# Optimization experiments

Measured on AMD Instinct MI355X. Metric: run time of the kernel, lower is better.

The kernel has to match this reference:

```python
import jax, jax.numpy as jnp
import numpy as np

B, S, D, H = 2, 4096, 512, 8
DK = D // H


def setup_inputs() -> dict:
    key = jax.random.key(0)
    ks = jax.random.split(key, 8)
    q = jax.random.normal(ks[0], (B, S, D), dtype=jnp.float32)
    k = jax.random.normal(ks[1], (B, S, D), dtype=jnp.float32)
    v = jax.random.normal(ks[2], (B, S, D), dtype=jnp.float32)
    mask = jax.random.randint(ks[3], (B, S, S), 0, 2, dtype=jnp.int32)
    scale = 1.0 / np.sqrt(D)
    w_q = jax.random.normal(ks[4], (D, D), dtype=jnp.float32) * scale
    w_k = jax.random.normal(ks[5], (D, D), dtype=jnp.float32) * scale
    w_v = jax.random.normal(ks[6], (D, D), dtype=jnp.float32) * scale
    w_o = jax.random.normal(ks[7], (D, D), dtype=jnp.float32) * scale
    return {"q": q, "k": k, "v": v, "mask": mask,
            "w_q": w_q, "w_k": w_k, "w_v": w_v, "w_o": w_o}


def reference(q, k, v, mask, w_q, w_k, w_v, w_o):
    # Projections (weights stored as [in, out]; no bias, matching bias=False)
    # [B,S,D] -> [B,H,S,DK]
    def split_heads(x):
        return x.reshape(B, S, H, DK).transpose(0, 2, 1, 3)

    qh = split_heads(q @ w_q)
    kh = split_heads(k @ w_k)
    vh = split_heads(v @ w_v)

    inv_sqrt_dk = jnp.float32(1.0 / np.sqrt(DK))
    # Explicit O(S^2) score matrix, as in the original module
    scores = jnp.einsum('bhqd,bhkd->bhqk', qh, kh) * inv_sqrt_dk
    scores = jnp.where(mask[:, None, :, :] == 0, jnp.float32(-1e9), scores)
    attn = jax.nn.softmax(scores, axis=-1)
    # dropout in eval mode (p=0) -> identity
    x = jnp.einsum('bhqk,bhkd->bhqd', attn, vh)
    x = x.transpose(0, 2, 1, 3).reshape(B, S, D)
    return x @ w_o
```

## Files before the change

### kernel.cpp

```cpp
#include <hip/hip_runtime.h>
#include <hip/hip_bf16.h>

#define Bn 2
#define Sn 4096
#define Dn 512
#define Hn 8
#define DKn 64

typedef __attribute__((ext_vector_type(8))) short bf16x8;
typedef __attribute__((ext_vector_type(4))) float f32x4;
typedef __attribute__((ext_vector_type(4))) _Float16 f16x4;
typedef __attribute__((ext_vector_type(8))) unsigned short us8;
typedef __attribute__((ext_vector_type(4))) unsigned short us4;

__device__ __forceinline__ unsigned short f2bf(float f) {
  unsigned u = __builtin_bit_cast(unsigned, f);
  u += 0x7fffu + ((u >> 16) & 1u);
  return (unsigned short)(u >> 16);
}

__global__ __launch_bounds__(256) void pack_mask_k(const int* __restrict__ mask,
                                                   unsigned int* __restrict__ pm) {
  int gid = blockIdx.x * 256 + threadIdx.x;
  int m = mask[gid];
  unsigned long long bal = __ballot(m != 0);
  if ((threadIdx.x & 63) == 0) {
    int q = (gid >> 12) & 4095;
    int b = gid >> 24;
    int kvw = (gid >> 5) & 127;
    pm[((size_t)b * 128 + kvw) * 4096 + q] = (unsigned)bal;
    pm[((size_t)b * 128 + kvw + 1) * 4096 + q] = (unsigned)(bal >> 32);
  }
}

__global__ __launch_bounds__(256) void cvt_k(const float* __restrict__ q,
                                             const float* __restrict__ k,
                                             const float* __restrict__ v,
                                             unsigned short* __restrict__ o) {
  const float* src = blockIdx.y == 0 ? q : blockIdx.y == 1 ? k : v;
  size_t i = (size_t)blockIdx.x * 256 + threadIdx.x;
  float4 f = *(const float4*)&src[i * 4];
  us4 r = {f2bf(f.x), f2bf(f.y), f2bf(f.z), f2bf(f.w)};
  *(us4*)&o[(size_t)blockIdx.y * (Bn * Sn * Dn) + i * 4] = r;
}

__global__ __launch_bounds__(256) void wt_k(const float* __restrict__ wq,
                                            const float* __restrict__ wk,
                                            const float* __restrict__ wv,
                                            const float* __restrict__ wo,
                                            unsigned short* __restrict__ wt) {
  __shared__ unsigned short ls[64][68];
  const float* W = blockIdx.z == 0 ? wq : blockIdx.z == 1 ? wk
                 : blockIdx.z == 2 ? wv : wo;
  int k0 = blockIdx.x * 64, n0 = blockIdx.y * 64;
  int t = threadIdx.x;
  for (int j = 0; j < 4; ++j) {
    int i = t + j * 256;
    int r = i >> 4, c4 = (i & 15) << 2;
    float4 f = *(const float4*)&W[(size_t)(k0 + r) * 512 + n0 + c4];
    ls[c4 + 0][r] = f2bf(f.x);
    ls[c4 + 1][r] = f2bf(f.y);
    ls[c4 + 2][r] = f2bf(f.z);
    ls[c4 + 3][r] = f2bf(f.w);
  }
  __syncthreads();
  unsigned short* out = wt + (size_t)blockIdx.z * 512 * 512;
  for (int j = 0; j < 4; ++j) {
    int i = t + j * 256;
    int r = i >> 4, c4 = (i & 15) << 2;
    us4 v = {ls[r][c4], ls[r][c4 + 1], ls[r][c4 + 2], ls[r][c4 + 3]};
    *(us4*)&out[(size_t)(n0 + r) * 512 + k0 + c4] = v;
  }
}

template <int MT, bool HEADS>
__global__ __launch_bounds__(256, 2) void gemm_k(
    const unsigned short* __restrict__ A0, size_t zstride,
    const unsigned short* __restrict__ wt, unsigned short* __restrict__ oh,
    unsigned short* __restrict__ vtg, float* __restrict__ olin) {
  __shared__ unsigned short As[MT * 64 * 64];
  __shared__ unsigned short Bs[128 * 64];
  const int z = blockIdx.z;
  const unsigned short* A = A0 + zstride * z;
  const unsigned short* Wt = wt + (size_t)z * 512 * 512;
  const float scale = (HEADS && z == 0) ? 0.125f * 1.44269504088896f : 1.0f;
  const int m0 = blockIdx.x * (MT * 64), n0 = blockIdx.y * 128;
  const int t = threadIdx.x, w = t >> 6, l = t & 63;
  const int quad = l >> 4, c = l & 15;

  f32x4 acc[MT][8] = {};

  us8 apre[MT * 2], bpre[4];
#pragma unroll
  for (int j = 0; j < MT * 2; ++j) {
    int i = t + j * 256, r = i >> 3, u = i & 7;
    apre[j] = *(const us8*)&A[(size_t)(m0 + r) * 512 + (u << 3)];
  }
#pragma unroll
  for (int j = 0; j < 4; ++j) {
    int i = t + j * 256, r = i >> 3, u = i & 7;
    bpre[j] = *(const us8*)&Wt[(size_t)(n0 + r) * 512 + (u << 3)];
  }

  for (int k0 = 0; k0 < 512; k0 += 64) {
    __syncthreads();
#pragma unroll
    for (int j = 0; j < MT * 2; ++j) {
      int i = t + j * 256, r = i >> 3, u = i & 7;
      *(us8*)&As[r * 64 + ((u ^ (r & 7)) << 3)] = apre[j];
    }
#pragma unroll
    for (int j = 0; j < 4; ++j) {
      int i = t + j * 256, r = i >> 3, u = i & 7;
      *(us8*)&Bs[r * 64 + ((u ^ (r & 7)) << 3)] = bpre[j];
    }
    __syncthreads();
    if (k0 + 64 < 512) {
#pragma unroll
      for (int j = 0; j < MT * 2; ++j) {
        int i = t + j * 256, r = i >> 3, u = i & 7;
        apre[j] = *(const us8*)&A[(size_t)(m0 + r) * 512 + k0 + 64 + (u << 3)];
      }
#pragma unroll
      for (int j = 0; j < 4; ++j) {
        int i = t + j * 256, r = i >> 3, u = i & 7;
        bpre[j] = *(const us8*)&Wt[(size_t)(n0 + r) * 512 + k0 + 64 + (u << 3)];
      }
    }

#pragma unroll
    for (int kc = 0; kc < 2; ++kc) {
      bf16x8 aA[MT], bB[8];
      int u = kc * 4 + quad;
#pragma unroll
      for (int mt = 0; mt < MT; ++mt) {
        int row = w * (MT * 16) + mt * 16 + c;
        aA[mt] = *(const bf16x8*)&As[row * 64 + ((u ^ (c & 7)) << 3)];
      }
#pragma unroll
      for (int nt = 0; nt < 8; ++nt) {
        int row = nt * 16 + c;
        bB[nt] = *(const bf16x8*)&Bs[row * 64 + ((u ^ (c & 7)) << 3)];
      }
#pragma unroll
      for (int mt = 0; mt < MT; ++mt)
#pragma unroll
        for (int nt = 0; nt < 8; ++nt)
          acc[mt][nt] = __builtin_amdgcn_mfma_f32_16x16x32_bf16(
              aA[mt], bB[nt], acc[mt][nt], 0, 0, 0);
    }
  }

#pragma unroll
  for (int mt = 0; mt < MT; ++mt)
#pragma unroll
    for (int nt = 0; nt < 8; ++nt)
#pragma unroll
      for (int r = 0; r < 4; ++r) {
        int m = m0 + w * (MT * 16) + mt * 16 + (quad << 2) + r;
        int n = n0 + nt * 16 + c;
        float val = acc[mt][nt][r] * scale;
        if constexpr (HEADS) {
          int b = m >> 12, s = m & 4095, h = n >> 6, dk = n & 63;
          if (z < 2) {
            oh[(size_t)z * (Bn * Hn * Sn * DKn) +
               ((size_t)(b * Hn + h) * Sn + s) * DKn + dk] = f2bf(val);
          } else {
            int sl = s & 63;
            int pos = (((sl >> 5) & 1) << 5) | (((sl >> 2) & 3) << 3) |
                      (((sl >> 4) & 1) << 2) | (sl & 3);
            vtg[((size_t)(b * Hn + h) * DKn + dk) * Sn + (s & ~63) + pos] =
                __builtin_bit_cast(unsigned short, (_Float16)val);
          }
        } else {
          olin[(size_t)m * 512 + n] = val;
        }
      }
}

__global__ __launch_bounds__(256, 2) void flash_k(
    const unsigned short* __restrict__ Qh, const unsigned short* __restrict__ Kh,
    const unsigned short* __restrict__ VtG, const unsigned int* __restrict__ pmt,
    unsigned short* __restrict__ attn) {
  __shared__ unsigned short Ks[64 * 64];
  __shared__ unsigned short Vts[64 * 64];
  __shared__ unsigned int Mw[256];

  const int q0 = blockIdx.x * 128, h = blockIdx.y, b = blockIdx.z;
  const int t = threadIdx.x, w = t >> 6, l = t & 63;
  const int quad = l >> 4, c = l & 15;
  const size_t hb = (size_t)(b * Hn + h) * Sn * DKn;
  const unsigned short* Qg = Qh + hb;
  const unsigned short* Kg = Kh + hb;
  const unsigned short* Vg = VtG + hb;

  bf16x8 bQ[2][2];
#pragma unroll
  for (int qf = 0; qf < 2; ++qf) {
    int qrow = q0 + w * 32 + qf * 16 + c;
#pragma unroll
    for (int kc = 0; kc < 2; ++kc)
      bQ[qf][kc] = *(const bf16x8*)&Qg[(size_t)qrow * 64 + kc * 32 + quad * 8];
  }

  f32x4 oacc[2][4] = {};
  float lsum[2] = {};
  const int sr = t >> 3, su = t & 7;

  us8 kpre[2], vpre[2];
  unsigned mpre;
#pragma unroll
  for (int j = 0; j < 2; ++j) {
    kpre[j] = *(const us8*)&Kg[(size_t)(sr + j * 32) * 64 + (su << 3)];
    vpre[j] = *(const us8*)&Vg[(size_t)(sr + j * 32) * Sn + (su << 3)];
  }
  mpre = pmt[((size_t)b * 128 + (t >> 7)) * 4096 + q0 + (t & 127)];

  for (int kv0 = 0; kv0 < Sn; kv0 += 64) {
    __syncthreads();
#pragma unroll
    for (int j = 0; j < 2; ++j) {
      int r = sr + j * 32;
      *(us8*)&Ks[r * 64 + ((su ^ (r & 7)) << 3)] = kpre[j];
      *(us8*)&Vts[r * 64 + ((su ^ (r & 7)) << 3)] = vpre[j];
    }
    Mw[t] = mpre;
    __syncthreads();
    if (kv0 + 64 < Sn) {
#pragma unroll
      for (int j = 0; j < 2; ++j) {
        kpre[j] = *(const us8*)&Kg[(size_t)(kv0 + 64 + sr + j * 32) * 64 + (su << 3)];
        vpre[j] = *(const us8*)&Vg[(size_t)(sr + j * 32) * Sn + kv0 + 64 + (su << 3)];
      }
      mpre = pmt[((size_t)b * 128 + ((kv0 + 64) >> 5) + (t >> 7)) * 4096 +
                 q0 + (t & 127)];
    }

    f32x4 sacc[2][4] = {};
#pragma unroll
    for (int kc = 0; kc < 2; ++kc) {
      int u = kc * 4 + quad;
#pragma unroll
      for (int kvt = 0; kvt < 4; ++kvt) {
        int row = kvt * 16 + c;
        bf16x8 aK = *(const bf16x8*)&Ks[row * 64 + ((u ^ (c & 7)) << 3)];
#pragma unroll
        for (int qf = 0; qf < 2; ++qf)
          sacc[qf][kvt] = __builtin_amdgcn_mfma_f32_16x16x32_bf16(
              aK, bQ[qf][kc], sacc[qf][kvt], 0, 0, 0);
      }
    }

    f16x4 pb[2][4];
#pragma unroll
    for (int qf = 0; qf < 2; ++qf) {
      int qloc = w * 32 + qf * 16 + c;
      unsigned mv0 = Mw[qloc], mv1 = Mw[128 + qloc];
#pragma unroll
      for (int kvt = 0; kvt < 4; ++kvt) {
        unsigned word = (kvt & 2) ? mv1 : mv0;
        unsigned bits = (word >> (((kvt & 1) << 4) + (quad << 2))) & 15u;
        float ps = 0.f;
#pragma unroll
        for (int r = 0; r < 4; ++r) {
          float p = ((bits >> r) & 1u) ? __builtin_amdgcn_exp2f(sacc[qf][kvt][r])
                                       : 0.f;
          ps += p;
          pb[qf][kvt][r] = (_Float16)p;
        }
        lsum[qf] += ps;
      }
    }

#pragma unroll
    for (int kp = 0; kp < 2; ++kp) {
#pragma unroll
      for (int dkt = 0; dkt < 4; ++dkt) {
        int dk = dkt * 16 + c;
        us8 vv = *(const us8*)&Vts[dk * 64 + (((kp * 4 + quad) ^ (c & 7)) << 3)];
        f16x4 lo = __builtin_bit_cast(f16x4, (us4){vv[0], vv[1], vv[2], vv[3]});
        f16x4 hi = __builtin_bit_cast(f16x4, (us4){vv[4], vv[5], vv[6], vv[7]});
#pragma unroll
        for (int qf = 0; qf < 2; ++qf) {
          oacc[qf][dkt] = __builtin_amdgcn_mfma_f32_16x16x16f16(
              pb[qf][kp * 2], lo, oacc[qf][dkt], 0, 0, 0);
          oacc[qf][dkt] = __builtin_amdgcn_mfma_f32_16x16x16f16(
              pb[qf][kp * 2 + 1], hi, oacc[qf][dkt], 0, 0, 0);
        }
      }
    }
  }

#pragma unroll
  for (int qf = 0; qf < 2; ++qf) {
    float s = lsum[qf];
    s += __shfl_xor(s, 16, 64);
    s += __shfl_xor(s, 32, 64);
    float inv = 1.0f / s;
#pragma unroll
    for (int r = 0; r < 4; ++r) {
      float invr = __shfl(inv, (quad << 2) + r, 64);
      unsigned short* dst =
          &attn[((size_t)(b * Sn + q0 + w * 32 + qf * 16 + (quad << 2) + r)) * Dn +
                h * 64 + c];
#pragma unroll
      for (int dkt = 0; dkt < 4; ++dkt)
        dst[dkt * 16] = f2bf(oacc[qf][dkt][r] * invr);
    }
  }
}

extern "C" void kernel_launch(void* const* d_in, const int* in_sizes, int n_in,
                              void* d_out, int out_size, void* d_ws,
                              size_t ws_size, hipStream_t stream) {
  const float* q = (const float*)d_in[0];
  const float* k = (const float*)d_in[1];
  const float* v = (const float*)d_in[2];
  const int* mask = (const int*)d_in[3];
  const float* wq = (const float*)d_in[4];
  const float* wk = (const float*)d_in[5];
  const float* wv = (const float*)d_in[6];
  const float* wo = (const float*)d_in[7];
  float* out = (float*)d_out;

  char* ws = (char*)d_ws;
  const size_t headN = (size_t)Bn * Hn * Sn * DKn;
  const size_t tensB = headN * 2;
  unsigned short* qbkb = (unsigned short*)ws;
  unsigned short* attn = (unsigned short*)ws;
  size_t off = 3 * tensB;
  unsigned short* qkv = (unsigned short*)(ws + off);
  off += 3 * tensB;
  unsigned short* wt = (unsigned short*)(ws + off);
  off += 4ull * 512 * 512 * 2;
  unsigned int* pm = (unsigned int*)(ws + off);

  pack_mask_k<<<(Bn * Sn * Sn) / 256, 256, 0, stream>>>(mask, pm);
  cvt_k<<<dim3(4096, 3), 256, 0, stream>>>(q, k, v, qbkb);
  wt_k<<<dim3(8, 8, 4), 256, 0, stream>>>(wq, wk, wv, wo, wt);
  gemm_k<2, true><<<dim3(64, 4, 3), 256, 0, stream>>>(
      qbkb, headN, wt, qkv, qkv + 2 * headN, nullptr);
  flash_k<<<dim3(32, 8, 2), 256, 0, stream>>>(qkv, qkv + headN,
                                              qkv + 2 * headN, pm, attn);
  gemm_k<1, false><<<dim3(128, 4, 1), 256, 0, stream>>>(
      attn, 0, wt + 3ull * 512 * 512, nullptr, nullptr, out);
}
```

Measured before the change: 420.2 us.

## Double-buffer LDS tiles in GEMM and flash kernels; coalesce V transpose store

Both the projection GEMM and the flash attention kernel now keep two LDS buffers. Each step writes the next tile into the alternate buffer after its compute, which cuts the per-iteration barriers from two to one so global loads and LDS writes overlap with MFMA work. The V projection epilogue now stages the transposed, permuted f16 tile through shared memory and writes it to global memory as 16-byte vectors instead of scattered 2-byte stores. The cost is more LDS per block, which may lower occupancy, and extra register pressure while the prefetched data is held.

```diff
diff --git a/kernel.cpp b/kernel.cpp
--- a/kernel.cpp
+++ b/kernel.cpp
@@ -78,8 +78,7 @@
     const unsigned short* __restrict__ A0, size_t zstride,
     const unsigned short* __restrict__ wt, unsigned short* __restrict__ oh,
     unsigned short* __restrict__ vtg, float* __restrict__ olin) {
-  __shared__ unsigned short As[MT * 64 * 64];
-  __shared__ unsigned short Bs[128 * 64];
+  __shared__ unsigned short smem[MT * 8192 + 16384];
   const int z = blockIdx.z;
   const unsigned short* A = A0 + zstride * z;
   const unsigned short* Wt = wt + (size_t)z * 512 * 512;
@@ -89,8 +88,8 @@
   const int quad = l >> 4, c = l & 15;
 
   f32x4 acc[MT][8] = {};
-
   us8 apre[MT * 2], bpre[4];
+
 #pragma unroll
   for (int j = 0; j < MT * 2; ++j) {
     int i = t + j * 256, r = i >> 3, u = i & 7;
@@ -101,21 +100,24 @@
     int i = t + j * 256, r = i >> 3, u = i & 7;
     bpre[j] = *(const us8*)&Wt[(size_t)(n0 + r) * 512 + (u << 3)];
   }
+#pragma unroll
+  for (int j = 0; j < MT * 2; ++j) {
+    int i = t + j * 256, r = i >> 3, u = i & 7;
+    *(us8*)&smem[r * 64 + ((u ^ (r & 7)) << 3)] = apre[j];
+  }
+#pragma unroll
+  for (int j = 0; j < 4; ++j) {
+    int i = t + j * 256, r = i >> 3, u = i & 7;
+    *(us8*)&smem[MT * 8192 + r * 64 + ((u ^ (r & 7)) << 3)] = bpre[j];
+  }
 
   for (int k0 = 0; k0 < 512; k0 += 64) {
+    const int cur = (k0 >> 6) & 1;
+    const unsigned short* AsC = &smem[cur * (MT * 4096)];
+    const unsigned short* BsC = &smem[MT * 8192 + cur * 8192];
     __syncthreads();
-#pragma unroll
-    for (int j = 0; j < MT * 2; ++j) {
-      int i = t + j * 256, r = i >> 3, u = i & 7;
-      *(us8*)&As[r * 64 + ((u ^ (r & 7)) << 3)] = apre[j];
-    }
-#pragma unroll
-    for (int j = 0; j < 4; ++j) {
-      int i = t + j * 256, r = i >> 3, u = i & 7;
-      *(us8*)&Bs[r * 64 + ((u ^ (r & 7)) << 3)] = bpre[j];
-    }
-    __syncthreads();
-    if (k0 + 64 < 512) {
+    const bool nxt = k0 + 64 < 512;
+    if (nxt) {
 #pragma unroll
       for (int j = 0; j < MT * 2; ++j) {
         int i = t + j * 256, r = i >> 3, u = i & 7;
@@ -135,12 +137,12 @@
 #pragma unroll
       for (int mt = 0; mt < MT; ++mt) {
         int row = w * (MT * 16) + mt * 16 + c;
-        aA[mt] = *(const bf16x8*)&As[row * 64 + ((u ^ (c & 7)) << 3)];
+        aA[mt] = *(const bf16x8*)&AsC[row * 64 + ((u ^ (c & 7)) << 3)];
       }
 #pragma unroll
       for (int nt = 0; nt < 8; ++nt) {
         int row = nt * 16 + c;
-        bB[nt] = *(const bf16x8*)&Bs[row * 64 + ((u ^ (c & 7)) << 3)];
+        bB[nt] = *(const bf16x8*)&BsC[row * 64 + ((u ^ (c & 7)) << 3)];
       }
 #pragma unroll
       for (int mt = 0; mt < MT; ++mt)
@@ -149,42 +151,87 @@
           acc[mt][nt] = __builtin_amdgcn_mfma_f32_16x16x32_bf16(
               aA[mt], bB[nt], acc[mt][nt], 0, 0, 0);
     }
-  }
-
-#pragma unroll
-  for (int mt = 0; mt < MT; ++mt)
-#pragma unroll
-    for (int nt = 0; nt < 8; ++nt)
-#pragma unroll
-      for (int r = 0; r < 4; ++r) {
-        int m = m0 + w * (MT * 16) + mt * 16 + (quad << 2) + r;
-        int n = n0 + nt * 16 + c;
-        float val = acc[mt][nt][r] * scale;
-        if constexpr (HEADS) {
-          int b = m >> 12, s = m & 4095, h = n >> 6, dk = n & 63;
-          if (z < 2) {
+
+    if (nxt) {
+      unsigned short* AsN = &smem[(cur ^ 1) * (MT * 4096)];
+      unsigned short* BsN = &smem[MT * 8192 + (cur ^ 1) * 8192];
+#pragma unroll
+      for (int j = 0; j < MT * 2; ++j) {
+        int i = t + j * 256, r = i >> 3, u = i & 7;
+        *(us8*)&AsN[r * 64 + ((u ^ (r & 7)) << 3)] = apre[j];
+      }
+#pragma unroll
+      for (int j = 0; j < 4; ++j) {
+        int i = t + j * 256, r = i >> 3, u = i & 7;
+        *(us8*)&BsN[r * 64 + ((u ^ (r & 7)) << 3)] = bpre[j];
+      }
+    }
+  }
+
+  if constexpr (HEADS) {
+    if (z == 2) {
+      __syncthreads();
+#pragma unroll
+      for (int mt = 0; mt < MT; ++mt) {
+        int mb = w * (MT * 16) + mt * 16 + (quad << 2);
+        int ml = (mb & 64) | (((mb >> 5) & 1) << 5) | (((mb >> 2) & 3) << 3) |
+                 (((mb >> 4) & 1) << 2);
+#pragma unroll
+        for (int nt = 0; nt < 8; ++nt) {
+          int nl = nt * 16 + c;
+          us4 pk;
+#pragma unroll
+          for (int r = 0; r < 4; ++r)
+            pk[r] = __builtin_bit_cast(unsigned short, (_Float16)acc[mt][nt][r]);
+          *(us4*)&smem[nl * 152 + ml] = pk;
+        }
+      }
+      __syncthreads();
+      const int bb = m0 >> 12, sb = m0 & 4095;
+#pragma unroll
+      for (int j = 0; j < MT * 4; ++j) {
+        int i = t + j * 256;
+        int nl = i >> 4, mc = (i & 15) << 3;
+        us8 vv = *(const us8*)&smem[nl * 152 + mc];
+        int n = n0 + nl, hh = n >> 6, dk = n & 63;
+        *(us8*)&vtg[((size_t)(bb * Hn + hh) * DKn + dk) * Sn + sb + mc] = vv;
+      }
+    } else {
+#pragma unroll
+      for (int mt = 0; mt < MT; ++mt)
+#pragma unroll
+        for (int nt = 0; nt < 8; ++nt)
+#pragma unroll
+          for (int r = 0; r < 4; ++r) {
+            int m = m0 + w * (MT * 16) + mt * 16 + (quad << 2) + r;
+            int n = n0 + nt * 16 + c;
+            int b = m >> 12, s = m & 4095, hh = n >> 6, dk = n & 63;
             oh[(size_t)z * (Bn * Hn * Sn * DKn) +
-               ((size_t)(b * Hn + h) * Sn + s) * DKn + dk] = f2bf(val);
-          } else {
-            int sl = s & 63;
-            int pos = (((sl >> 5) & 1) << 5) | (((sl >> 2) & 3) << 3) |
-                      (((sl >> 4) & 1) << 2) | (sl & 3);
-            vtg[((size_t)(b * Hn + h) * DKn + dk) * Sn + (s & ~63) + pos] =
-                __builtin_bit_cast(unsigned short, (_Float16)val);
+               ((size_t)(b * Hn + hh) * Sn + s) * DKn + dk] =
+                f2bf(acc[mt][nt][r] * scale);
           }
-        } else {
-          olin[(size_t)m * 512 + n] = val;
+    }
+  } else {
+#pragma unroll
+    for (int mt = 0; mt < MT; ++mt)
+#pragma unroll
+      for (int nt = 0; nt < 8; ++nt)
+#pragma unroll
+        for (int r = 0; r < 4; ++r) {
+          int m = m0 + w * (MT * 16) + mt * 16 + (quad << 2) + r;
+          int n = n0 + nt * 16 + c;
+          olin[(size_t)m * 512 + n] = acc[mt][nt][r];
         }
-      }
+  }
 }
 
 __global__ __launch_bounds__(256, 2) void flash_k(
     const unsigned short* __restrict__ Qh, const unsigned short* __restrict__ Kh,
     const unsigned short* __restrict__ VtG, const unsigned int* __restrict__ pmt,
     unsigned short* __restrict__ attn) {
-  __shared__ unsigned short Ks[64 * 64];
-  __shared__ unsigned short Vts[64 * 64];
-  __shared__ unsigned int Mw[256];
+  __shared__ unsigned short Ks[2][64 * 64];
+  __shared__ unsigned short Vts[2][64 * 64];
+  __shared__ unsigned int Mw[2][256];
 
   const int q0 = blockIdx.x * 128, h = blockIdx.y, b = blockIdx.z;
   const int t = threadIdx.x, w = t >> 6, l = t & 63;
@@ -206,32 +253,31 @@
   f32x4 oacc[2][4] = {};
   float lsum[2] = {};
   const int sr = t >> 3, su = t & 7;
+  const int off0 = sr * 64 + ((su ^ (sr & 7)) << 3);
+  const int off1 = (sr + 32) * 64 + ((su ^ (sr & 7)) << 3);
 
   us8 kpre[2], vpre[2];
   unsigned mpre;
-#pragma unroll
-  for (int j = 0; j < 2; ++j) {
-    kpre[j] = *(const us8*)&Kg[(size_t)(sr + j * 32) * 64 + (su << 3)];
-    vpre[j] = *(const us8*)&Vg[(size_t)(sr + j * 32) * Sn + (su << 3)];
-  }
+  kpre[0] = *(const us8*)&Kg[(size_t)sr * 64 + (su << 3)];
+  kpre[1] = *(const us8*)&Kg[(size_t)(sr + 32) * 64 + (su << 3)];
+  vpre[0] = *(const us8*)&Vg[(size_t)sr * Sn + (su << 3)];
+  vpre[1] = *(const us8*)&Vg[(size_t)(sr + 32) * Sn + (su << 3)];
   mpre = pmt[((size_t)b * 128 + (t >> 7)) * 4096 + q0 + (t & 127)];
+  *(us8*)&Ks[0][off0] = kpre[0];
+  *(us8*)&Ks[0][off1] = kpre[1];
+  *(us8*)&Vts[0][off0] = vpre[0];
+  *(us8*)&Vts[0][off1] = vpre[1];
+  Mw[0][t] = mpre;
 
   for (int kv0 = 0; kv0 < Sn; kv0 += 64) {
+    const int cur = (kv0 >> 6) & 1;
     __syncthreads();
-#pragma unroll
-    for (int j = 0; j < 2; ++j) {
-      int r = sr + j * 32;
-      *(us8*)&Ks[r * 64 + ((su ^ (r & 7)) << 3)] = kpre[j];
-      *(us8*)&Vts[r * 64 + ((su ^ (r & 7)) << 3)] = vpre[j];
-    }
-    Mw[t] = mpre;
-    __syncthreads();
-    if (kv0 + 64 < Sn) {
-#pragma unroll
-      for (int j = 0; j < 2; ++j) {
-        kpre[j] = *(const us8*)&Kg[(size_t)(kv0 + 64 + sr + j * 32) * 64 + (su << 3)];
-        vpre[j] = *(const us8*)&Vg[(size_t)(sr + j * 32) * Sn + kv0 + 64 + (su << 3)];
-      }
+    const bool nxt = kv0 + 64 < Sn;
+    if (nxt) {
+      kpre[0] = *(const us8*)&Kg[(size_t)(kv0 + 64 + sr) * 64 + (su << 3)];
+      kpre[1] = *(const us8*)&Kg[(size_t)(kv0 + 96 + sr) * 64 + (su << 3)];
+      vpre[0] = *(const us8*)&Vg[(size_t)sr * Sn + kv0 + 64 + (su << 3)];
+      vpre[1] = *(const us8*)&Vg[(size_t)(sr + 32) * Sn + kv0 + 64 + (su << 3)];
       mpre = pmt[((size_t)b * 128 + ((kv0 + 64) >> 5) + (t >> 7)) * 4096 +
                  q0 + (t & 127)];
     }
@@ -243,7 +289,7 @@
 #pragma unroll
       for (int kvt = 0; kvt < 4; ++kvt) {
         int row = kvt * 16 + c;
-        bf16x8 aK = *(const bf16x8*)&Ks[row * 64 + ((u ^ (c & 7)) << 3)];
+        bf16x8 aK = *(const bf16x8*)&Ks[cur][row * 64 + ((u ^ (c & 7)) << 3)];
 #pragma unroll
         for (int qf = 0; qf < 2; ++qf)
           sacc[qf][kvt] = __builtin_amdgcn_mfma_f32_16x16x32_bf16(
@@ -255,7 +301,7 @@
 #pragma unroll
     for (int qf = 0; qf < 2; ++qf) {
       int qloc = w * 32 + qf * 16 + c;
-      unsigned mv0 = Mw[qloc], mv1 = Mw[128 + qloc];
+      unsigned mv0 = Mw[cur][qloc], mv1 = Mw[cur][128 + qloc];
 #pragma unroll
       for (int kvt = 0; kvt < 4; ++kvt) {
         unsigned word = (kvt & 2) ? mv1 : mv0;
@@ -277,7 +323,8 @@
 #pragma unroll
       for (int dkt = 0; dkt < 4; ++dkt) {
         int dk = dkt * 16 + c;
-        us8 vv = *(const us8*)&Vts[dk * 64 + (((kp * 4 + quad) ^ (c & 7)) << 3)];
+        us8 vv = *(const us8*)&Vts[cur][dk * 64 +
+                                        (((kp * 4 + quad) ^ (c & 7)) << 3)];
         f16x4 lo = __builtin_bit_cast(f16x4, (us4){vv[0], vv[1], vv[2], vv[3]});
         f16x4 hi = __builtin_bit_cast(f16x4, (us4){vv[4], vv[5], vv[6], vv[7]});
 #pragma unroll
@@ -288,6 +335,15 @@
               pb[qf][kp * 2 + 1], hi, oacc[qf][dkt], 0, 0, 0);
         }
       }
+    }
+
+    if (nxt) {
+      const int nb = cur ^ 1;
+      *(us8*)&Ks[nb][off0] = kpre[0];
+      *(us8*)&Ks[nb][off1] = kpre[1];
+      *(us8*)&Vts[nb][off0] = vpre[0];
+      *(us8*)&Vts[nb][off1] = vpre[1];
+      Mw[nb][t] = mpre;
     }
   }
 
```

Result: faster. 409.4 us (-2.6%).
